# Kernel tuning notes

Measured on AMD Instinct MI355X. Metric: run time of the kernel, lower is better.

## Reference

```python
import jax, jax.numpy as jnp
import numpy as np

NM, ND = 50000, 50000          # mirna / disease node counts
DM, DD = 256, 256              # m_sim / d_sim feature dims
F = 64                         # feature_attn_size
E = 1600000                    # number of edges (avg degree 16)
N = NM + ND
SLOPE = 0.2                    # leaky_relu negative slope


def setup_inputs() -> dict:
    key = jax.random.key(0)
    k1, k2, k3, k4, k5, k6 = jax.random.split(key, 6)
    return {
        "m_sim": jax.random.normal(k1, (NM, DM), dtype=jnp.float32),
        "d_sim": jax.random.normal(k2, (ND, DD), dtype=jnp.float32),
        "Wm": jax.random.normal(k3, (F, DM), dtype=jnp.float32) / np.sqrt(DM).astype(np.float32),
        "Wd": jax.random.normal(k4, (F, DD), dtype=jnp.float32) / np.sqrt(DD).astype(np.float32),
        "src": jax.random.randint(k5, (E,), 0, N),
        "dst": jax.random.randint(k6, (E,), 0, N),
    }


def reference(m_sim, d_sim, Wm, Wd, src, dst):
    # node projection (dropout omitted: eval mode). mirna nodes first, then disease nodes.
    z = jnp.concatenate([m_sim @ Wm.T, d_sim @ Wd.T], axis=0)  # [N, F]

    # edge attention score: dot(z_src, z_dst) then leaky_relu
    z_src = z[src]                                             # [E, F] gather
    e = jnp.sum(z_src * z[dst], axis=1)                        # [E]
    e = jax.nn.leaky_relu(e, SLOPE)

    # segment softmax over incoming edges of each dst node (numerically stable)
    emax = jax.ops.segment_max(e, dst, num_segments=N)         # [N]
    emax = jnp.where(jnp.isfinite(emax), emax, 0.0)            # isolated nodes
    ex = jnp.exp(e - emax[dst])                                # [E]
    denom = jax.ops.segment_sum(ex, dst, num_segments=N)       # [N]
    alpha = ex / denom[dst]                                    # [E]

    # weighted aggregation + elu (isolated nodes get h=0, elu(0)=0)
    h = jax.ops.segment_sum(alpha[:, None] * z_src, dst, num_segments=N)  # [N, F]
    return jax.nn.elu(h)
```

## Files before the change

### kernel.cpp

```cpp
#include <hip/hip_runtime.h>
#include <math.h>

#define NM 50000
#define ND 50000
#define NN 100000
#define DK 256
#define F  64
#define SLOPE 0.2f

#define NBZ   391
#define NPROJ (NBZ * 2)

#define NBUCK 391
#define BCAP  8192
#define CH    4096
#define QCAP  2048

typedef short bf16x8 __attribute__((ext_vector_type(8)));
typedef float f32x4  __attribute__((ext_vector_type(4)));

__device__ __forceinline__ void cvt8(const float4& a0, const float4& a1,
                                     bf16x8& hi, bf16x8& lo) {
    float v[8] = {a0.x, a0.y, a0.z, a0.w, a1.x, a1.y, a1.z, a1.w};
    #pragma unroll
    for (int e = 0; e < 8; ++e) {
        unsigned u  = __float_as_uint(v[e]);
        unsigned r  = u + 0x7FFF + ((u >> 16) & 1);
        unsigned short hb = (unsigned short)(r >> 16);
        float hf = __uint_as_float(((unsigned)hb) << 16);
        float lf = v[e] - hf;
        unsigned ul = __float_as_uint(lf);
        unsigned rl = ul + 0x7FFF + ((ul >> 16) & 1);
        hi[e] = (short)hb;
        lo[e] = (short)(rl >> 16);
    }
}

__global__ __launch_bounds__(512, 1) void fused1(const float* __restrict__ m_sim,
                                                 const float* __restrict__ d_sim,
                                                 const float* __restrict__ Wm,
                                                 const float* __restrict__ Wd,
                                                 float* __restrict__ z,
                                                 const int* __restrict__ src,
                                                 const int* __restrict__ dst,
                                                 int* __restrict__ pkb_g,
                                                 int* __restrict__ bcur,
                                                 int nchunks, int E) {
    __shared__ __align__(16) char smem[65536];
    int t = threadIdx.x;

    if ((int)blockIdx.x < nchunks) {
        int* cnt   = (int*)smem;
        int* scx   = cnt + 512;
        int* lcur  = scx + 512;
        int* gbase = lcur + 512;
        int* pkb_l = gbase + 512;
        int* bkt_l = pkb_l + CH;

        int base = blockIdx.x * CH;
        int chunkN = E - base; if (chunkN > CH) chunkN = CH;

        cnt[t] = 0;
        __syncthreads();

        int ss[8], ds[8];
        #pragma unroll
        for (int e = 0; e < 8; ++e) {
            int k = base + e * 512 + t;
            if (e * 512 + t < chunkN) {
                ds[e] = dst[k];
                ss[e] = src[k];
                atomicAdd(&cnt[ds[e] >> 8], 1);
            }
        }
        __syncthreads();

        int x = cnt[t];
        scx[t] = x;
        __syncthreads();
        for (int off = 1; off < 512; off <<= 1) {
            int v = (t >= off) ? scx[t - off] : 0;
            __syncthreads();
            scx[t] += v;
            __syncthreads();
        }
        int lexcl = scx[t] - x;
        scx[t] = lexcl;
        lcur[t] = lexcl;
        gbase[t] = atomicAdd(&bcur[t], x);
        __syncthreads();

        #pragma unroll
        for (int e = 0; e < 8; ++e) {
            if (e * 512 + t < chunkN) {
                int b = ds[e] >> 8;
                int p = atomicAdd(&lcur[b], 1);
                pkb_l[p] = (ss[e] << 8) | (ds[e] & 255);
                bkt_l[p] = b;
            }
        }
        __syncthreads();

        for (int idx = t; idx < chunkN; idx += 512) {
            int b = bkt_l[idx];
            int g = b * BCAP + gbase[b] + (idx - scx[b]);
            pkb_g[g] = pkb_l[idx];
        }
        return;
    }

    short* Whi = (short*)smem;
    short* Wlo = (short*)(smem + 32768);

    int bid  = blockIdx.x - nchunks;
    bool ism = bid < NBZ;
    const float* sim = ism ? m_sim : d_sim;
    const float* W   = ism ? Wm : Wd;
    int row0   = (ism ? bid : bid - NBZ) * 128;
    int nrows  = ism ? NM : ND;
    int zbase  = ism ? 0 : NM;

    int l = t & 63;
    int w = t >> 6;
    int frow = l & 15;
    int kg   = l >> 4;

    int grow = row0 + w * 16 + frow; if (grow > nrows - 1) grow = nrows - 1;
    const float4* ap = (const float4*)(sim + (size_t)grow * DK) + kg * 2;

    float4 pa0 = ap[0], pa1 = ap[1];
    float4 pb0 = ap[8], pb1 = ap[9];

    {
        int r = t >> 3;
        int q = t & 7;
        const float4* wr = (const float4*)(W + (size_t)r * DK);
        #pragma unroll
        for (int i = 0; i < 4; ++i) {
            int ls = q * 4 + i;
            float4 b0 = wr[ls * 2], b1 = wr[ls * 2 + 1];
            bf16x8 hi, lo;
            cvt8(b0, b1, hi, lo);
            int ps = ls ^ (r & 7);
            *(bf16x8*)&Whi[r * 256 + ps * 8] = hi;
            *(bf16x8*)&Wlo[r * 256 + ps * 8] = lo;
        }
    }
    __syncthreads();

    f32x4 acc[4];
    #pragma unroll
    for (int j = 0; j < 4; ++j) acc[j] = (f32x4){0.f, 0.f, 0.f, 0.f};

    #pragma unroll 1
    for (int step = 0; step < 8; ++step) {
        bf16x8 ahi, alo;
        cvt8(pa0, pa1, ahi, alo);
        pa0 = pb0; pa1 = pb1;
        if (step + 2 < 8) {
            pb0 = ap[(step + 2) * 8];
            pb1 = ap[(step + 2) * 8 + 1];
        }

        int ls = step * 4 + kg;
        #pragma unroll
        for (int j = 0; j < 4; ++j) {
            int wrow = j * 16 + frow;
            int ps = ls ^ (wrow & 7);
            bf16x8 bhi = *(const bf16x8*)&Whi[wrow * 256 + ps * 8];
            bf16x8 blo = *(const bf16x8*)&Wlo[wrow * 256 + ps * 8];
            acc[j] = __builtin_amdgcn_mfma_f32_16x16x32_bf16(ahi, bhi, acc[j], 0, 0, 0);
            acc[j] = __builtin_amdgcn_mfma_f32_16x16x32_bf16(ahi, blo, acc[j], 0, 0, 0);
            acc[j] = __builtin_amdgcn_mfma_f32_16x16x32_bf16(alo, bhi, acc[j], 0, 0, 0);
        }
    }

    #pragma unroll
    for (int j = 0; j < 4; ++j) {
        #pragma unroll
        for (int reg = 0; reg < 4; ++reg) {
            int r = row0 + w * 16 + kg * 4 + reg;
            if (r < nrows)
                z[((zbase + r) << 6) + j * 16 + frow] = acc[j][reg];
        }
    }
}

__global__ __launch_bounds__(256) void gat2(const float* __restrict__ z,
                                            const int* __restrict__ pkb_g,
                                            const int* __restrict__ bcur,
                                            float* __restrict__ out) {
    __shared__ int dcnt[64], loc[64], lcur[64];
    __shared__ int csr_l[QCAP];

    int t  = threadIdx.x;
    int b  = blockIdx.x >> 2;
    int q  = blockIdx.x & 3;
    int node0 = (b << 8) + (q << 6);
    int nbe = bcur[b];
    const int* pp = pkb_g + (size_t)b * BCAP;

    if (t < 64) dcnt[t] = 0;
    __syncthreads();
    for (int i = t; i < nbe; i += 256) {
        int pk = pp[i];
        if (((pk >> 6) & 3) == q) atomicAdd(&dcnt[pk & 63], 1);
    }
    __syncthreads();
    if (t < 64) loc[t] = dcnt[t];
    __syncthreads();
    for (int off = 1; off < 64; off <<= 1) {
        int v = (t < 64 && t >= off) ? loc[t - off] : 0;
        __syncthreads();
        if (t < 64) loc[t] += v;
        __syncthreads();
    }
    if (t < 64) { int e0 = loc[t] - dcnt[t]; loc[t] = e0; lcur[t] = e0; }
    __syncthreads();
    for (int i = t; i < nbe; i += 256) {
        int pk = pp[i];
        if (((pk >> 6) & 3) == q) {
            int pos = atomicAdd(&lcur[pk & 63], 1);
            csr_l[pos] = pk >> 8;
        }
    }
    __syncthreads();

    int lane = t & 63;
    int w    = t >> 6;
    int g    = lane >> 4;
    int i4   = lane & 15;
    int iq   = i4 << 2;

    for (int nn_ = 0; nn_ < 16; ++nn_) {
        int n    = w * 16 + nn_;
        int node = node0 + n;
        if (node >= NN) break;
        int beg = loc[n];
        int end = beg + dcnt[n];

        float4 zd = *(const float4*)(z + (node << 6) + iq);
        float  m = -1e30f, ssum = 0.f;
        float4 h = {0.f, 0.f, 0.f, 0.f};

        for (int j = beg; j < end; j += 16) {
            int   off_[4];
            bool  val[4];
            float4 v[4];
            float p[4], e[4], ex[4];
            #pragma unroll
            for (int k = 0; k < 4; ++k) {
                int jj = j + k * 4 + g;
                val[k] = jj < end;
                off_[k] = (csr_l[val[k] ? jj : beg] << 6) + iq;
            }
            #pragma unroll
            for (int k = 0; k < 4; ++k)
                v[k] = *(const float4*)(z + off_[k]);
            #pragma unroll
            for (int k = 0; k < 4; ++k)
                p[k] = v[k].x * zd.x + v[k].y * zd.y + v[k].z * zd.z + v[k].w * zd.w;
            #pragma unroll
            for (int o = 1; o < 16; o <<= 1) {
                #pragma unroll
                for (int k = 0; k < 4; ++k) p[k] += __shfl_xor(p[k], o, 64);
            }
            #pragma unroll
            for (int k = 0; k < 4; ++k) {
                float ek = (p[k] > 0.f) ? p[k] : SLOPE * p[k];
                e[k] = val[k] ? ek : -1e30f;
            }
            float nm = fmaxf(m, fmaxf(fmaxf(e[0], e[1]), fmaxf(e[2], e[3])));
            float sc = __expf(m - nm);
            #pragma unroll
            for (int k = 0; k < 4; ++k) ex[k] = val[k] ? __expf(e[k] - nm) : 0.f;
            ssum = ssum * sc + ex[0] + ex[1] + ex[2] + ex[3];
            h.x = h.x * sc + ex[0] * v[0].x + ex[1] * v[1].x + ex[2] * v[2].x + ex[3] * v[3].x;
            h.y = h.y * sc + ex[0] * v[0].y + ex[1] * v[1].y + ex[2] * v[2].y + ex[3] * v[3].y;
            h.z = h.z * sc + ex[0] * v[0].z + ex[1] * v[1].z + ex[2] * v[2].z + ex[3] * v[3].z;
            h.w = h.w * sc + ex[0] * v[0].w + ex[1] * v[1].w + ex[2] * v[2].w + ex[3] * v[3].w;
            m = nm;
        }

        float M = fmaxf(m, __shfl_xor(m, 16, 64));
        M = fmaxf(M, __shfl_xor(M, 32, 64));
        float sc = __expf(m - M);
        float ss = ssum * sc;
        ss += __shfl_xor(ss, 16, 64);
        ss += __shfl_xor(ss, 32, 64);
        h.x *= sc; h.y *= sc; h.z *= sc; h.w *= sc;
        h.x += __shfl_xor(h.x, 16, 64); h.x += __shfl_xor(h.x, 32, 64);
        h.y += __shfl_xor(h.y, 16, 64); h.y += __shfl_xor(h.y, 32, 64);
        h.z += __shfl_xor(h.z, 16, 64); h.z += __shfl_xor(h.z, 32, 64);
        h.w += __shfl_xor(h.w, 16, 64); h.w += __shfl_xor(h.w, 32, 64);

        if (g == 0) {
            float rs = 1.0f / ss;
            bool has = end > beg;
            float4 o;
            o.x = has ? h.x * rs : 0.f;
            o.y = has ? h.y * rs : 0.f;
            o.z = has ? h.z * rs : 0.f;
            o.w = has ? h.w * rs : 0.f;
            o.x = (o.x > 0.f) ? o.x : (__expf(o.x) - 1.f);
            o.y = (o.y > 0.f) ? o.y : (__expf(o.y) - 1.f);
            o.z = (o.z > 0.f) ? o.z : (__expf(o.z) - 1.f);
            o.w = (o.w > 0.f) ? o.w : (__expf(o.w) - 1.f);
            *(float4*)(out + (node << 6) + iq) = o;
        }
    }
}

extern "C" void kernel_launch(void* const* d_in, const int* in_sizes, int n_in,
                              void* d_out, int out_size, void* d_ws, size_t ws_size,
                              hipStream_t stream) {
    const float* m_sim = (const float*)d_in[0];
    const float* d_sim = (const float*)d_in[1];
    const float* Wm    = (const float*)d_in[2];
    const float* Wd    = (const float*)d_in[3];
    const int*   src   = (const int*)d_in[4];
    const int*   dst   = (const int*)d_in[5];
    int E = in_sizes[4];
    float* out = (float*)d_out;

    char* ws = (char*)d_ws;
    float* z      = (float*)ws; ws += (size_t)NN * F * 4;
    int*   bcur   = (int*)ws;   ws += 512 * 4;
    int*   pkb_g  = (int*)ws;   ws += (size_t)NBUCK * BCAP * 4;

    hipMemsetAsync(bcur, 0, 512 * 4, stream);

    int nchunks = (E + CH - 1) / CH;
    fused1<<<nchunks + NPROJ, 512, 0, stream>>>(m_sim, d_sim, Wm, Wd, z,
                                                src, dst, pkb_g, bcur, nchunks, E);
    gat2<<<NBUCK * 4, 256, 0, stream>>>(z, pkb_g, bcur, out);
}
```

Before: 125.1 us.

## Bucket edges by 64-node groups so each gat2 block reads only its edges

The edge binning in the first kernel now uses 1563 buckets of 64 destination nodes instead of 391 buckets of 256 nodes. Each thread scans 4 bucket counts and the atomic reservation on the global cursor is skipped for empty buckets. The aggregation kernel then maps one block to one bucket, so it no longer reads the whole 256-node bucket four times and filters by quarter. The cost is more global buckets, more atomics and smaller per-bucket capacity (2048), which could overflow on skewed degree distributions.

```diff
diff --git a/kernel.cpp b/kernel.cpp
--- a/kernel.cpp
+++ b/kernel.cpp
@@ -11,10 +11,10 @@
 #define NBZ   391
 #define NPROJ (NBZ * 2)
 
-#define NBUCK 391
-#define BCAP  8192
+#define NB64  1563
+#define QBCAP 2048
 #define CH    4096
-#define QCAP  2048
+#define NPAD  2048
 
 typedef short bf16x8 __attribute__((ext_vector_type(8)));
 typedef float f32x4  __attribute__((ext_vector_type(4)));
@@ -51,16 +51,17 @@
 
     if ((int)blockIdx.x < nchunks) {
         int* cnt   = (int*)smem;
-        int* scx   = cnt + 512;
-        int* lcur  = scx + 512;
-        int* gbase = lcur + 512;
-        int* pkb_l = gbase + 512;
+        int* lcur  = cnt + NPAD;
+        int* gbase = lcur + NPAD;
+        int* sp    = gbase + NPAD;
+        int* pkb_l = sp + 512;
         int* bkt_l = pkb_l + CH;
 
         int base = blockIdx.x * CH;
         int chunkN = E - base; if (chunkN > CH) chunkN = CH;
 
-        cnt[t] = 0;
+        #pragma unroll
+        for (int e = 0; e < 4; ++e) cnt[e * 512 + t] = 0;
         __syncthreads();
 
         int ss[8], ds[8];
@@ -70,32 +71,38 @@
             if (e * 512 + t < chunkN) {
                 ds[e] = dst[k];
                 ss[e] = src[k];
-                atomicAdd(&cnt[ds[e] >> 8], 1);
-            }
-        }
-        __syncthreads();
-
-        int x = cnt[t];
-        scx[t] = x;
+                atomicAdd(&cnt[ds[e] >> 6], 1);
+            }
+        }
+        __syncthreads();
+
+        int c4[4], run = 0;
+        #pragma unroll
+        for (int e = 0; e < 4; ++e) { c4[e] = cnt[t * 4 + e]; run += c4[e]; }
+        sp[t] = run;
         __syncthreads();
         for (int off = 1; off < 512; off <<= 1) {
-            int v = (t >= off) ? scx[t - off] : 0;
+            int v = (t >= off) ? sp[t - off] : 0;
             __syncthreads();
-            scx[t] += v;
+            sp[t] += v;
             __syncthreads();
         }
-        int lexcl = scx[t] - x;
-        scx[t] = lexcl;
-        lcur[t] = lexcl;
-        gbase[t] = atomicAdd(&bcur[t], x);
+        int texcl = sp[t] - run;
+        #pragma unroll
+        for (int e = 0; e < 4; ++e) {
+            int b = t * 4 + e;
+            lcur[b] = texcl;
+            gbase[b] = (c4[e] > 0) ? atomicAdd(&bcur[b], c4[e]) : 0;
+            texcl += c4[e];
+        }
         __syncthreads();
 
         #pragma unroll
         for (int e = 0; e < 8; ++e) {
             if (e * 512 + t < chunkN) {
-                int b = ds[e] >> 8;
+                int b = ds[e] >> 6;
                 int p = atomicAdd(&lcur[b], 1);
-                pkb_l[p] = (ss[e] << 8) | (ds[e] & 255);
+                pkb_l[p] = (ss[e] << 6) | (ds[e] & 63);
                 bkt_l[p] = b;
             }
         }
@@ -103,7 +110,7 @@
 
         for (int idx = t; idx < chunkN; idx += 512) {
             int b = bkt_l[idx];
-            int g = b * BCAP + gbase[b] + (idx - scx[b]);
+            int g = b * QBCAP + gbase[b] + (idx - (lcur[b] - cnt[b]));
             pkb_g[g] = pkb_l[idx];
         }
         return;
@@ -191,38 +198,33 @@
                                             const int* __restrict__ bcur,
                                             float* __restrict__ out) {
     __shared__ int dcnt[64], loc[64], lcur[64];
-    __shared__ int csr_l[QCAP];
+    __shared__ int csr_l[QBCAP];
 
     int t  = threadIdx.x;
-    int b  = blockIdx.x >> 2;
-    int q  = blockIdx.x & 3;
-    int node0 = (b << 8) + (q << 6);
+    int b  = blockIdx.x;
+    int node0 = b << 6;
     int nbe = bcur[b];
-    const int* pp = pkb_g + (size_t)b * BCAP;
+    const int* pp = pkb_g + (size_t)b * QBCAP;
 
     if (t < 64) dcnt[t] = 0;
+    __syncthreads();
+    for (int i = t; i < nbe; i += 256)
+        atomicAdd(&dcnt[pp[i] & 63], 1);
+    __syncthreads();
+    if (t < 64) loc[t] = dcnt[t];
+    __syncthreads();
+    for (int off = 1; off < 64; off <<= 1) {
+        int v = (t < 64 && t >= off) ? loc[t - off] : 0;
+        __syncthreads();
+        if (t < 64) loc[t] += v;
+        __syncthreads();
+    }
+    if (t < 64) { int e0 = loc[t] - dcnt[t]; loc[t] = e0; lcur[t] = e0; }
     __syncthreads();
     for (int i = t; i < nbe; i += 256) {
         int pk = pp[i];
-        if (((pk >> 6) & 3) == q) atomicAdd(&dcnt[pk & 63], 1);
-    }
-    __syncthreads();
-    if (t < 64) loc[t] = dcnt[t];
-    __syncthreads();
-    for (int off = 1; off < 64; off <<= 1) {
-        int v = (t < 64 && t >= off) ? loc[t - off] : 0;
-        __syncthreads();
-        if (t < 64) loc[t] += v;
-        __syncthreads();
-    }
-    if (t < 64) { int e0 = loc[t] - dcnt[t]; loc[t] = e0; lcur[t] = e0; }
-    __syncthreads();
-    for (int i = t; i < nbe; i += 256) {
-        int pk = pp[i];
-        if (((pk >> 6) & 3) == q) {
-            int pos = atomicAdd(&lcur[pk & 63], 1);
-            csr_l[pos] = pk >> 8;
-        }
+        int pos = atomicAdd(&lcur[pk & 63], 1);
+        csr_l[pos] = pk >> 6;
     }
     __syncthreads();
 
@@ -325,13 +327,13 @@
 
     char* ws = (char*)d_ws;
     float* z      = (float*)ws; ws += (size_t)NN * F * 4;
-    int*   bcur   = (int*)ws;   ws += 512 * 4;
-    int*   pkb_g  = (int*)ws;   ws += (size_t)NBUCK * BCAP * 4;
-
-    hipMemsetAsync(bcur, 0, 512 * 4, stream);
+    int*   bcur   = (int*)ws;   ws += NPAD * 4;
+    int*   pkb_g  = (int*)ws;   ws += (size_t)NB64 * QBCAP * 4;
+
+    hipMemsetAsync(bcur, 0, NPAD * 4, stream);
 
     int nchunks = (E + CH - 1) / CH;
     fused1<<<nchunks + NPROJ, 512, 0, stream>>>(m_sim, d_sim, Wm, Wd, z,
                                                 src, dst, pkb_g, bcur, nchunks, E);
-    gat2<<<NBUCK * 4, 256, 0, stream>>>(z, pkb_g, bcur, out);
+    gat2<<<NB64, 256, 0, stream>>>(z, pkb_g, bcur, out);
 }
```

New measurement: 144.6 us. 15.7% more time.

## Split each dst bucket into halves with 512-thread blocks and register-cached edge reads

Applied to the files above, without the earlier changes.

The aggregation kernel now gives each bucket of 256 destination nodes to two 512-thread blocks covering 128 nodes each, where it used four 256-thread blocks covering 64 nodes each. Each bucket's packed edge list is therefore read twice from global memory, down from four times. Each thread also holds its up to 16 edges in registers, so the counting and scatter passes no longer reload them. In exchange the edge loop is fixed at 16×512 entries, which relies on BCAP=8192, and the local CSR capacity grows to 3072. The unseen per-node loop must handle 8 waves × 16 nodes for this to be correct.

```diff
diff --git a/kernel.cpp b/kernel.cpp
--- a/kernel.cpp
+++ b/kernel.cpp
@@ -14,7 +14,7 @@
 #define NBUCK 391
 #define BCAP  8192
 #define CH    4096
-#define QCAP  2048
+#define HCAP  3072
 
 typedef short bf16x8 __attribute__((ext_vector_type(8)));
 typedef float f32x4  __attribute__((ext_vector_type(4)));
@@ -186,42 +186,53 @@
     }
 }
 
-__global__ __launch_bounds__(256) void gat2(const float* __restrict__ z,
-                                            const int* __restrict__ pkb_g,
-                                            const int* __restrict__ bcur,
-                                            float* __restrict__ out) {
-    __shared__ int dcnt[64], loc[64], lcur[64];
-    __shared__ int csr_l[QCAP];
+__global__ __launch_bounds__(512) void gat2h(const float* __restrict__ z,
+                                             const int* __restrict__ pkb_g,
+                                             const int* __restrict__ bcur,
+                                             float* __restrict__ out) {
+    __shared__ int dcnt[128], loc[128], lcur[128];
+    __shared__ int csr_l[HCAP];
 
     int t  = threadIdx.x;
-    int b  = blockIdx.x >> 2;
-    int q  = blockIdx.x & 3;
-    int node0 = (b << 8) + (q << 6);
+    int b  = blockIdx.x >> 1;
+    int hh = blockIdx.x & 1;
+    int node0 = (b << 8) + (hh << 7);
     int nbe = bcur[b];
     const int* pp = pkb_g + (size_t)b * BCAP;
 
-    if (t < 64) dcnt[t] = 0;
-    __syncthreads();
-    for (int i = t; i < nbe; i += 256) {
-        int pk = pp[i];
-        if (((pk >> 6) & 3) == q) atomicAdd(&dcnt[pk & 63], 1);
-    }
-    __syncthreads();
-    if (t < 64) loc[t] = dcnt[t];
-    __syncthreads();
-    for (int off = 1; off < 64; off <<= 1) {
-        int v = (t < 64 && t >= off) ? loc[t - off] : 0;
-        __syncthreads();
-        if (t < 64) loc[t] += v;
-        __syncthreads();
-    }
-    if (t < 64) { int e0 = loc[t] - dcnt[t]; loc[t] = e0; lcur[t] = e0; }
-    __syncthreads();
-    for (int i = t; i < nbe; i += 256) {
-        int pk = pp[i];
-        if (((pk >> 6) & 3) == q) {
-            int pos = atomicAdd(&lcur[pk & 63], 1);
-            csr_l[pos] = pk >> 8;
+    if (t < 128) dcnt[t] = 0;
+    __syncthreads();
+
+    int ed[16]; bool kv[16];
+    #pragma unroll
+    for (int e = 0; e < 16; ++e) {
+        int i = e * 512 + t;
+        bool v = i < nbe;
+        int pk = v ? pp[i] : 0;
+        kv[e] = v && (((pk >> 7) & 1) == hh);
+        ed[e] = pk;
+    }
+    #pragma unroll
+    for (int e = 0; e < 16; ++e)
+        if (kv[e]) atomicAdd(&dcnt[ed[e] & 127], 1);
+    __syncthreads();
+
+    if (t < 128) loc[t] = dcnt[t];
+    __syncthreads();
+    for (int off = 1; off < 128; off <<= 1) {
+        int v = (t < 128 && t >= off) ? loc[t - off] : 0;
+        __syncthreads();
+        if (t < 128) loc[t] += v;
+        __syncthreads();
+    }
+    if (t < 128) { int e0 = loc[t] - dcnt[t]; loc[t] = e0; lcur[t] = e0; }
+    __syncthreads();
+
+    #pragma unroll
+    for (int e = 0; e < 16; ++e) {
+        if (kv[e]) {
+            int pos = atomicAdd(&lcur[ed[e] & 127], 1);
+            csr_l[pos] = ed[e] >> 8;
         }
     }
     __syncthreads();
@@ -333,5 +344,5 @@
     int nchunks = (E + CH - 1) / CH;
     fused1<<<nchunks + NPROJ, 512, 0, stream>>>(m_sim, d_sim, Wm, Wd, z,
                                                 src, dst, pkb_g, bcur, nchunks, E);
-    gat2<<<NBUCK * 4, 256, 0, stream>>>(z, pkb_g, bcur, out);
+    gat2h<<<NBUCK * 2, 512, 0, stream>>>(z, pkb_g, bcur, out);
 }
```

Result: no change. 125.0 us (-0.0%).
